# Performance work log

Hardware: AMD Instinct MI355X
Metric: run time of the kernel (lower is better)

## Reference

```python
import jax, jax.numpy as jnp
import numpy as np

EPS = 1e-8


def setup_inputs() -> dict:
    key = jax.random.key(0)
    k1, k2, k3, k4, k5 = jax.random.split(key, 5)
    B, N_LOG, N_PHYS, E = 16, 512, 2048, 2048
    P = jax.random.uniform(k1, (B, N_LOG, N_PHYS), dtype=jnp.float32)
    d_hw = jax.random.randint(k2, (N_PHYS, N_PHYS), 0, 4, dtype=jnp.int32)
    edge_src = jax.random.randint(k3, (B, E), 0, N_LOG, dtype=jnp.int32)
    edge_dst = jax.random.randint(k4, (B, E), 0, N_LOG, dtype=jnp.int32)
    edge_w = jax.random.uniform(k5, (B, E), dtype=jnp.float32)
    return {"P": P, "d_hw": d_hw, "edge_src": edge_src,
            "edge_dst": edge_dst, "edge_w": edge_w}


def reference(P, d_hw, edge_src, edge_dst, edge_w):
    # A_hw[p,q] = 1 where hardware distance == 1 (adjacent qubits)
    A_hw = (d_hw == 1).astype(P.dtype)                      # [Q, Q]
    B = P.shape[0]
    # Dense contraction once per batch: PA[b,i,q] = sum_p P[b,i,p] A[p,q]
    PA = jnp.einsum('bip,pq->biq', P, A_hw)                 # [B, N, Q]
    b_idx = jnp.arange(B)[:, None]                          # [B, 1]
    gi = PA[b_idx, edge_src]                                # [B, E, Q]
    gj = P[b_idx, edge_dst]                                 # [B, E, Q]
    adj_score = jnp.einsum('beq,beq->be', gi, gj)           # [B, E]
    sample_adj = jnp.sum(edge_w * adj_score, axis=-1)       # [B]
    sample_weight = jnp.maximum(jnp.sum(edge_w, axis=-1), EPS)
    # every sample has edges -> valid_samples = B
    loss = -jnp.mean(sample_adj / sample_weight)
    return loss
```

## Files before the change

kernel.cpp:

```cpp
#include <hip/hip_runtime.h>
#include <hip/hip_bf16.h>

#define BATCH 16
#define NLOG 512
#define Q 2048
#define NEDGE 2048
#define M_TOT (BATCH * NLOG)
#define KB 2048

typedef float f32x4 __attribute__((ext_vector_type(4)));
typedef int i32x4 __attribute__((ext_vector_type(4)));
typedef int i32x8 __attribute__((ext_vector_type(8)));

__device__ __forceinline__ unsigned char to_e4m3(float f) {
    int pk = __builtin_amdgcn_cvt_pk_fp8_f32(f, f, 0, false);
    return (unsigned char)(pk & 0xff);
}

__global__ __launch_bounds__(256) void prep(const float* __restrict__ P,
                                            unsigned char* __restrict__ P8,
                                            const int* __restrict__ d_hw,
                                            unsigned char* __restrict__ A8t,
                                            const int* __restrict__ esrc,
                                            const int* __restrict__ edst,
                                            const float* __restrict__ ew,
                                            float* __restrict__ Wf32,
                                            float* __restrict__ sw,
                                            float* __restrict__ total,
                                            unsigned* __restrict__ counter) {
    const int t = threadIdx.x;
    int bid = blockIdx.x;
    if (bid < 8192) {
        int i = (bid * 256 + t) * 8;
        float4 v0 = *(const float4*)(P + i);
        float4 v1 = *(const float4*)(P + i + 4);
        int lo = 0, hi = 0;
        lo = __builtin_amdgcn_cvt_pk_fp8_f32(v0.x, v0.y, lo, false);
        lo = __builtin_amdgcn_cvt_pk_fp8_f32(v0.z, v0.w, lo, true);
        hi = __builtin_amdgcn_cvt_pk_fp8_f32(v1.x, v1.y, hi, false);
        hi = __builtin_amdgcn_cvt_pk_fp8_f32(v1.z, v1.w, hi, true);
        int2 st; st.x = lo; st.y = hi;
        *(int2*)(P8 + i) = st;
    } else if (bid < 12288) {
        bid -= 8192;
        __shared__ unsigned char tile[32][33];
        int q0 = (bid & 63) * 32;
        int p0 = (bid >> 6) * 32;
        int tx = t & 31;
        int ty = t >> 5;
        for (int s = 0; s < 32; s += 8) {
            int p = p0 + ty + s;
            int v = d_hw[(size_t)p * Q + q0 + tx];
            tile[ty + s][tx] = (v == 1) ? 0x38 : 0x00;
        }
        __syncthreads();
        for (int s = 0; s < 32; s += 8) {
            A8t[(size_t)(q0 + ty + s) * Q + p0 + tx] = tile[tx][ty + s];
        }
    } else {
        int b = bid - 12288;
        if (b == 0 && t == 0) { *total = 0.f; *counter = 0u; }
        float s = 0.f;
        float* Wb = Wf32 + (size_t)b * NLOG * NLOG;
        #pragma unroll
        for (int k = 0; k < 8; k++) {
            int e = b * NEDGE + k * 256 + t;
            float wg = ew[e];
            s += wg;
            atomicAdd(&Wb[esrc[e] * NLOG + edst[e]], wg);
        }
        #pragma unroll
        for (int off = 32; off > 0; off >>= 1) s += __shfl_xor(s, off);
        __shared__ float red[4];
        if ((t & 63) == 0) red[t >> 6] = s;
        __syncthreads();
        if (t == 0) sw[b] = red[0] + red[1] + red[2] + red[3];
    }
}

__global__ __launch_bounds__(256, 2) void gemm_bt8(const unsigned char* __restrict__ A,
                                                   const unsigned char* __restrict__ Bt,
                                                   unsigned char* __restrict__ PA8) {
    __shared__ unsigned char As[32768];
    __shared__ unsigned char Bs[16384];

    const int t = threadIdx.x;
    const int w = t >> 6;
    const int wr = w >> 1, wc = w & 1;
    const int l = t & 63;
    const int quad = l >> 4;
    const int lane16 = l & 15;

    const int m0 = blockIdx.x * 256;
    const int n0 = blockIdx.y * 128;

    const int s_row = t >> 3;
    const int s_off = (((t & 7) ^ (s_row & 7)) << 4);
    const int r7 = lane16 & 7;
    const int c0 = ((2 * quad) ^ r7) << 4;
    const int c1 = ((2 * quad + 1) ^ r7) << 4;

    f32x4 acc[8][4] = {};

    for (int k0 = 0; k0 < KB; k0 += 128) {
        #pragma unroll
        for (int c = 0; c < 8; c++) {
            const unsigned char* g = A + (size_t)(m0 + c * 32 + s_row) * KB + k0 + s_off;
            __builtin_amdgcn_global_load_lds(
                (const __attribute__((address_space(1))) void*)g,
                (__attribute__((address_space(3))) void*)(As + c * 4096 + w * 1024),
                16, 0, 0);
        }
        #pragma unroll
        for (int c = 0; c < 4; c++) {
            const unsigned char* g = Bt + (size_t)(n0 + c * 32 + s_row) * KB + k0 + s_off;
            __builtin_amdgcn_global_load_lds(
                (const __attribute__((address_space(1))) void*)g,
                (__attribute__((address_space(3))) void*)(Bs + c * 4096 + w * 1024),
                16, 0, 0);
        }
        __syncthreads();

        i32x8 bfr[4];
        #pragma unroll
        for (int j = 0; j < 4; j++) {
            int base = (wc * 64 + j * 16 + lane16) << 7;
            i32x4 lo = *(const i32x4*)(Bs + base + c0);
            i32x4 hi = *(const i32x4*)(Bs + base + c1);
            bfr[j] = __builtin_shufflevector(lo, hi, 0, 1, 2, 3, 4, 5, 6, 7);
        }
        #pragma unroll
        for (int i = 0; i < 8; i++) {
            int base = (wr * 128 + i * 16 + lane16) << 7;
            i32x4 lo = *(const i32x4*)(As + base + c0);
            i32x4 hi = *(const i32x4*)(As + base + c1);
            i32x8 af = __builtin_shufflevector(lo, hi, 0, 1, 2, 3, 4, 5, 6, 7);
            #pragma unroll
            for (int j = 0; j < 4; j++)
                acc[i][j] = __builtin_amdgcn_mfma_scale_f32_16x16x128_f8f6f4(
                    af, bfr[j], acc[i][j], 0, 0, 0, 127, 0, 127);
        }
        __syncthreads();
    }

    #pragma unroll
    for (int i = 0; i < 8; i++) {
        #pragma unroll
        for (int j = 0; j < 4; j++) {
            #pragma unroll
            for (int r = 0; r < 4; r++) {
                int row = m0 + wr * 128 + i * 16 + quad * 4 + r;
                int col = n0 + wc * 64 + j * 16 + lane16;
                PA8[(size_t)row * Q + col] = to_e4m3(acc[i][j][r] * (1.0f / 256.0f));
            }
        }
    }
}

__global__ __launch_bounds__(256, 2) void gemm_sw(const unsigned char* __restrict__ PA8,
                                                  const unsigned char* __restrict__ P8,
                                                  const float* __restrict__ Wf32,
                                                  const float* __restrict__ sw,
                                                  float* __restrict__ total,
                                                  unsigned* __restrict__ counter,
                                                  float* __restrict__ out) {
    __shared__ unsigned char As[8192];
    __shared__ unsigned char Bs[16384];

    const int t = threadIdx.x;
    const int w = t >> 6;
    const int wr = w >> 1, wc = w & 1;
    const int l = t & 63;
    const int quad = l >> 4;
    const int lane16 = l & 15;

    const int b = blockIdx.z;
    const int m0 = blockIdx.x * 64;
    const int n0 = blockIdx.y * 128;
    const unsigned char* A  = PA8 + (size_t)b * NLOG * Q;
    const unsigned char* Bt = P8  + (size_t)b * NLOG * Q;
    const float* Wb = Wf32 + (size_t)b * NLOG * NLOG;

    const int s_row = t >> 3;
    const int s_off = (((t & 7) ^ (s_row & 7)) << 4);
    const int r7 = lane16 & 7;
    const int c0 = ((2 * quad) ^ r7) << 4;
    const int c1 = ((2 * quad + 1) ^ r7) << 4;

    f32x4 acc[2][4] = {};

    for (int k0 = 0; k0 < KB; k0 += 128) {
        #pragma unroll
        for (int c = 0; c < 2; c++) {
            const unsigned char* g = A + (size_t)(m0 + c * 32 + s_row) * KB + k0 + s_off;
            __builtin_amdgcn_global_load_lds(
                (const __attribute__((address_space(1))) void*)g,
                (__attribute__((address_space(3))) void*)(As + c * 4096 + w * 1024),
                16, 0, 0);
        }
        #pragma unroll
        for (int c = 0; c < 4; c++) {
            const unsigned char* g = Bt + (size_t)(n0 + c * 32 + s_row) * KB + k0 + s_off;
            __builtin_amdgcn_global_load_lds(
                (const __attribute__((address_space(1))) void*)g,
                (__attribute__((address_space(3))) void*)(Bs + c * 4096 + w * 1024),
                16, 0, 0);
        }
        __syncthreads();

        i32x8 bfr[4];
        #pragma unroll
        for (int j = 0; j < 4; j++) {
            int base = (wc * 64 + j * 16 + lane16) << 7;
            i32x4 lo = *(const i32x4*)(Bs + base + c0);
            i32x4 hi = *(const i32x4*)(Bs + base + c1);
            bfr[j] = __builtin_shufflevector(lo, hi, 0, 1, 2, 3, 4, 5, 6, 7);
        }
        #pragma unroll
        for (int i = 0; i < 2; i++) {
            int base = (wr * 32 + i * 16 + lane16) << 7;
            i32x4 lo = *(const i32x4*)(As + base + c0);
            i32x4 hi = *(const i32x4*)(As + base + c1);
            i32x8 af = __builtin_shufflevector(lo, hi, 0, 1, 2, 3, 4, 5, 6, 7);
            #pragma unroll
            for (int j = 0; j < 4; j++)
                acc[i][j] = __builtin_amdgcn_mfma_scale_f32_16x16x128_f8f6f4(
                    af, bfr[j], acc[i][j], 0, 0, 0, 127, 0, 127);
        }
        __syncthreads();
    }

    float part = 0.f;
    #pragma unroll
    for (int i = 0; i < 2; i++) {
        #pragma unroll
        for (int r = 0; r < 4; r++) {
            int row = m0 + wr * 32 + i * 16 + quad * 4 + r;
            const float* wrow = Wb + (size_t)row * NLOG + n0 + wc * 64 + lane16;
            #pragma unroll
            for (int j = 0; j < 4; j++)
                part += wrow[j * 16] * acc[i][j][r];
        }
    }
    #pragma unroll
    for (int off = 32; off > 0; off >>= 1) part += __shfl_xor(part, off);
    __shared__ float red[4];
    if (l == 0) red[w] = part;
    __syncthreads();

    __shared__ unsigned done;
    if (t == 0) {
        float scale = 256.0f / (16.0f * fmaxf(sw[b], 1e-8f));
        atomicAdd(total, (red[0] + red[1] + red[2] + red[3]) * scale);
        __threadfence();
        done = atomicAdd(counter, 1u);
    }
    __syncthreads();
    if (t == 0 && done == 512 - 1) {
        __threadfence();
        out[0] = -atomicAdd(total, 0.0f);
    }
}

extern "C" void kernel_launch(void* const* d_in, const int* in_sizes, int n_in,
                              void* d_out, int out_size, void* d_ws, size_t ws_size,
                              hipStream_t stream) {
    const float* P    = (const float*)d_in[0];
    const int* d_hw   = (const int*)d_in[1];
    const int* esrc   = (const int*)d_in[2];
    const int* edst   = (const int*)d_in[3];
    const float* ew   = (const float*)d_in[4];
    float* out        = (float*)d_out;

    char* ws = (char*)d_ws;
    unsigned char* P8  = (unsigned char*)ws;
    unsigned char* A8t = (unsigned char*)(ws + 16777216);
    unsigned char* PA8 = (unsigned char*)(ws + 20971520);
    float* Wf32        = (float*)(ws + 37748736);
    float* sw          = (float*)(ws + 54525952);
    float* total       = (float*)(ws + 54525952 + 64);
    unsigned* counter  = (unsigned*)(ws + 54525952 + 128);

    hipMemsetAsync(Wf32, 0, 16777216, stream);
    prep<<<8192 + 4096 + 16, 256, 0, stream>>>(P, P8, d_hw, A8t, esrc, edst, ew,
                                               Wf32, sw, total, counter);
    gemm_bt8<<<dim3(M_TOT / 256, Q / 128), 256, 0, stream>>>(P8, A8t, PA8);
    gemm_sw<<<dim3(NLOG / 64, NLOG / 128, BATCH), 256, 0, stream>>>(
        PA8, P8, Wf32, sw, total, counter, out);
}
```

Before: 192.0 us.

## Fuse W zeroing into prep and split-K the weighted second GEMM

Removes the separate hipMemsetAsync of the 16 MB edge-weight matrix. Prep now launches 128 extra blocks, each zeroing a 64-row slice of W for one batch and then scattering only the edges whose source row falls in that slice. The second GEMM uses 128x128 tiles with a two-way K split (batch x2 in grid z), so each block does more MFMA work per B-tile load while the total block count stays the same. This trades one launch and its memset for redundant edge-index reads across the 8 slice blocks, and doubles the A shared-memory buffer, which may lower occupancy.

After: 183.9 us. -4.2%, faster.

```diff
diff --git a/kernel.cpp b/kernel.cpp
--- a/kernel.cpp
+++ b/kernel.cpp
@@ -57,18 +57,31 @@
         for (int s = 0; s < 32; s += 8) {
             A8t[(size_t)(q0 + ty + s) * Q + p0 + tx] = tile[tx][ty + s];
         }
+    } else if (bid < 12416) {
+        int bb = bid - 12288;
+        int b = bb >> 3;
+        int c = bb & 7;
+        float* Wb = Wf32 + (size_t)b * NLOG * NLOG;
+        float4 z = {0.f, 0.f, 0.f, 0.f};
+        float* base = Wb + c * 64 * NLOG;
+        #pragma unroll
+        for (int s = 0; s < 32; s++)
+            *(float4*)(base + (s * 256 + t) * 4) = z;
+        __syncthreads();
+        int lo = c * 64, hi = lo + 64;
+        #pragma unroll
+        for (int k = 0; k < 8; k++) {
+            int e = b * NEDGE + k * 256 + t;
+            int src = esrc[e];
+            if (src >= lo && src < hi)
+                atomicAdd(&Wb[src * NLOG + edst[e]], ew[e]);
+        }
     } else {
-        int b = bid - 12288;
+        int b = bid - 12416;
         if (b == 0 && t == 0) { *total = 0.f; *counter = 0u; }
         float s = 0.f;
-        float* Wb = Wf32 + (size_t)b * NLOG * NLOG;
-        #pragma unroll
-        for (int k = 0; k < 8; k++) {
-            int e = b * NEDGE + k * 256 + t;
-            float wg = ew[e];
-            s += wg;
-            atomicAdd(&Wb[esrc[e] * NLOG + edst[e]], wg);
-        }
+        #pragma unroll
+        for (int k = 0; k < 8; k++) s += ew[b * NEDGE + k * 256 + t];
         #pragma unroll
         for (int off = 32; off > 0; off >>= 1) s += __shfl_xor(s, off);
         __shared__ float red[4];
@@ -164,7 +177,7 @@
                                                   float* __restrict__ total,
                                                   unsigned* __restrict__ counter,
                                                   float* __restrict__ out) {
-    __shared__ unsigned char As[8192];
+    __shared__ unsigned char As[16384];
     __shared__ unsigned char Bs[16384];
 
     const int t = threadIdx.x;
@@ -174,8 +187,9 @@
     const int quad = l >> 4;
     const int lane16 = l & 15;
 
-    const int b = blockIdx.z;
-    const int m0 = blockIdx.x * 64;
+    const int b  = blockIdx.z >> 1;
+    const int kh = blockIdx.z & 1;
+    const int m0 = blockIdx.x * 128;
     const int n0 = blockIdx.y * 128;
     const unsigned char* A  = PA8 + (size_t)b * NLOG * Q;
     const unsigned char* Bt = P8  + (size_t)b * NLOG * Q;
@@ -187,11 +201,11 @@
     const int c0 = ((2 * quad) ^ r7) << 4;
     const int c1 = ((2 * quad + 1) ^ r7) << 4;
 
-    f32x4 acc[2][4] = {};
-
-    for (int k0 = 0; k0 < KB; k0 += 128) {
-        #pragma unroll
-        for (int c = 0; c < 2; c++) {
+    f32x4 acc[4][4] = {};
+
+    for (int k0 = kh * 1024; k0 < kh * 1024 + 1024; k0 += 128) {
+        #pragma unroll
+        for (int c = 0; c < 4; c++) {
             const unsigned char* g = A + (size_t)(m0 + c * 32 + s_row) * KB + k0 + s_off;
             __builtin_amdgcn_global_load_lds(
                 (const __attribute__((address_space(1))) void*)g,
@@ -217,8 +231,8 @@
             bfr[j] = __builtin_shufflevector(lo, hi, 0, 1, 2, 3, 4, 5, 6, 7);
         }
         #pragma unroll
-        for (int i = 0; i < 2; i++) {
-            int base = (wr * 32 + i * 16 + lane16) << 7;
+        for (int i = 0; i < 4; i++) {
+            int base = (wr * 64 + i * 16 + lane16) << 7;
             i32x4 lo = *(const i32x4*)(As + base + c0);
             i32x4 hi = *(const i32x4*)(As + base + c1);
             i32x8 af = __builtin_shufflevector(lo, hi, 0, 1, 2, 3, 4, 5, 6, 7);
@@ -232,10 +246,10 @@
 
     float part = 0.f;
     #pragma unroll
-    for (int i = 0; i < 2; i++) {
+    for (int i = 0; i < 4; i++) {
         #pragma unroll
         for (int r = 0; r < 4; r++) {
-            int row = m0 + wr * 32 + i * 16 + quad * 4 + r;
+            int row = m0 + wr * 64 + i * 16 + quad * 4 + r;
             const float* wrow = Wb + (size_t)row * NLOG + n0 + wc * 64 + lane16;
             #pragma unroll
             for (int j = 0; j < 4; j++)
@@ -281,10 +295,10 @@
     float* total       = (float*)(ws + 54525952 + 64);
     unsigned* counter  = (unsigned*)(ws + 54525952 + 128);
 
-    hipMemsetAsync(Wf32, 0, 16777216, stream);
-    prep<<<8192 + 4096 + 16, 256, 0, stream>>>(P, P8, d_hw, A8t, esrc, edst, ew,
-                                               Wf32, sw, total, counter);
+    prep<<<8192 + 4096 + 128 + 16, 256, 0, stream>>>(P, P8, d_hw, A8t, esrc,
+                                                     edst, ew, Wf32, sw,
+                                                     total, counter);
     gemm_bt8<<<dim3(M_TOT / 256, Q / 128), 256, 0, stream>>>(P8, A8t, PA8);
-    gemm_sw<<<dim3(NLOG / 64, NLOG / 128, BATCH), 256, 0, stream>>>(
+    gemm_sw<<<dim3(NLOG / 128, NLOG / 128, BATCH * 2), 256, 0, stream>>>(
         PA8, P8, Wf32, sw, total, counter, out);
 }
```
